# Optimization experiments

Hardware: AMD Instinct MI355X
Metric: run time of the kernel (lower is better)

Reference implementation:

```python
import jax, jax.numpy as jnp
import numpy as np

NEIGHBOR = 9
PAD = (NEIGHBOR - 1) // 2  # 4


def setup_inputs() -> dict:
    key = jax.random.key(0)
    k1, k2 = jax.random.split(key)
    B, C, H, W = 32, 3, 512, 512
    x = jax.random.normal(k1, (B, C, H, W), dtype=jnp.float32)
    p = jax.random.uniform(k2, (B, 1, H, W), dtype=jnp.float32)
    return {"x": x, "p": p}


def reference(x, p):
    # filter = ones(3, 3, 9, 9) / 9**2  (OIHW) — sums box mean over ALL 3 input
    # channels into each output channel, exactly as torch F.conv2d does here.
    filt = jnp.ones((3, 3, NEIGHBOR, NEIGHBOR), dtype=x.dtype) / (NEIGHBOR ** 2)
    mean_normal = jax.lax.conv_general_dilated(
        x, filt,
        window_strides=(1, 1),
        padding=[(PAD, PAD), (PAD, PAD)],
        dimension_numbers=("NCHW", "OIHW", "NCHW"),
    )
    return p * x + (1.0 - p) * mean_normal
```

## Files before the change

kernel.cpp:

```cpp
#include <hip/hip_runtime.h>


#define TX 64
#define TY 64
#define HALO 4
#define THW (TY + 2 * HALO)
#define TWW (TX + 2 * HALO)

__global__ __launch_bounds__(256) void reflection_fusion_kernel(
    const float* __restrict__ x, const float* __restrict__ p,
    float* __restrict__ out, int H, int W) {
  __shared__ __align__(16) float csum[THW][TWW];

  const int tid = threadIdx.x;
  const int b = blockIdx.z;
  const int x0 = blockIdx.x * TX;
  const int y0 = blockIdx.y * TY;
  const long HW = (long)H * W;
  const float* xb = x + (long)b * 3 * HW;
  const float* pb = p + (long)b * HW;
  float* ob = out + (long)b * 3 * HW;

  const int NCHUNK = THW * (TWW / 4);
#pragma unroll
  for (int pass = 0; pass < 6; ++pass) {
    int i = tid + pass * 256;
    if (i < NCHUNK) {
      int r = (unsigned)i / 18u;
      int j = i - r * 18;
      int gy = y0 + r - HALO;
      int gx = x0 + 4 * j - HALO;
      float4 s = make_float4(0.f, 0.f, 0.f, 0.f);
      if ((unsigned)gy < (unsigned)H && gx >= 0 && gx + 4 <= W) {
        const float* base = xb + (long)gy * W + gx;
        float4 a = *(const float4*)(base);
        float4 c1 = *(const float4*)(base + HW);
        float4 c2 = *(const float4*)(base + 2 * HW);
        s.x = a.x + c1.x + c2.x;
        s.y = a.y + c1.y + c2.y;
        s.z = a.z + c1.z + c2.z;
        s.w = a.w + c1.w + c2.w;
      }
      *(float4*)&csum[r][4 * j] = s;
    }
  }
  __syncthreads();

  const int cc = tid & 63;
  const int rg = tid >> 6;
  const int rbase = rg * 16;

  float h[24];
#pragma unroll
  for (int k = 0; k < 24; ++k) {
    const float* row = &csum[rbase + k][cc];
    float s = row[0];
#pragma unroll
    for (int d = 1; d < 9; ++d) s += row[d];
    h[k] = s;
  }

  const float inv81 = 1.0f / 81.0f;
  float s = 0.f;
#pragma unroll
  for (int k = 0; k < 9; ++k) s += h[k];

#pragma unroll
  for (int it = 0; it < 16; ++it) {
    if (it > 0) s += h[it + 8] - h[it - 1];
    int gy = y0 + rbase + it;
    long pix = (long)gy * W + (x0 + cc);
    float pv = pb[pix];
    float m = s * inv81;
    float om = 1.0f - pv;
    float v0 = xb[pix];
    float v1 = xb[HW + pix];
    float v2 = xb[2 * HW + pix];
    ob[pix] = pv * v0 + om * m;
    ob[HW + pix] = pv * v1 + om * m;
    ob[2 * HW + pix] = pv * v2 + om * m;
  }
}

extern "C" void kernel_launch(void* const* d_in, const int* in_sizes, int n_in,
                              void* d_out, int out_size, void* d_ws, size_t ws_size,
                              hipStream_t stream) {
  const float* x = (const float*)d_in[0];
  const float* p = (const float*)d_in[1];
  float* out = (float*)d_out;

  const int H = 512, W = 512;
  const int B = in_sizes[1] / (H * W);

  dim3 grid(W / TX, H / TY, B);
  dim3 block(256);
  reflection_fusion_kernel<<<grid, block, 0, stream>>>(x, p, out, H, W);
}
```

Measured before the change: 215.6 us.

## Use wide 256x16 tiles with float4 outputs and sliding horizontal box sums

The tile shape changes from 64x64 to 256 wide by 16 tall, and each thread now produces 4 adjacent columns over 4 rows instead of 1 column over 16 rows. Horizontal 9-tap sums are read as float4 from LDS and computed with a sliding window, and p, x and out are accessed with float4 global loads and stores. The aim is fewer global memory instructions, less LDS traffic and a cheaper horizontal sum. The cost is a larger relative halo (24 rows per 16 output rows), shorter vertical reuse, and 8-column left/right halo padding in LDS.

```diff
diff --git a/kernel.cpp b/kernel.cpp
--- a/kernel.cpp
+++ b/kernel.cpp
@@ -1,16 +1,15 @@
 #include <hip/hip_runtime.h>
 
 
-#define TX 64
-#define TY 64
-#define HALO 4
-#define THW (TY + 2 * HALO)
-#define TWW (TX + 2 * HALO)
+#define TX 256
+#define TY 16
+#define CROWS (TY + 8)
+#define CCOLS 272
 
 __global__ __launch_bounds__(256) void reflection_fusion_kernel(
     const float* __restrict__ x, const float* __restrict__ p,
     float* __restrict__ out, int H, int W) {
-  __shared__ __align__(16) float csum[THW][TWW];
+  __shared__ __align__(16) float csum[CROWS][CCOLS];
 
   const int tid = threadIdx.x;
   const int b = blockIdx.z;
@@ -21,64 +20,75 @@
   const float* pb = p + (long)b * HW;
   float* ob = out + (long)b * 3 * HW;
 
-  const int NCHUNK = THW * (TWW / 4);
-#pragma unroll
-  for (int pass = 0; pass < 6; ++pass) {
-    int i = tid + pass * 256;
-    if (i < NCHUNK) {
-      int r = (unsigned)i / 18u;
-      int j = i - r * 18;
-      int gy = y0 + r - HALO;
-      int gx = x0 + 4 * j - HALO;
-      float4 s = make_float4(0.f, 0.f, 0.f, 0.f);
-      if ((unsigned)gy < (unsigned)H && gx >= 0 && gx + 4 <= W) {
-        const float* base = xb + (long)gy * W + gx;
-        float4 a = *(const float4*)(base);
-        float4 c1 = *(const float4*)(base + HW);
-        float4 c2 = *(const float4*)(base + 2 * HW);
-        s.x = a.x + c1.x + c2.x;
-        s.y = a.y + c1.y + c2.y;
-        s.z = a.z + c1.z + c2.z;
-        s.w = a.w + c1.w + c2.w;
-      }
-      *(float4*)&csum[r][4 * j] = s;
+  for (int i = tid; i < CROWS * 68; i += 256) {
+    int r = (unsigned)i / 68u;
+    int k = i - r * 68;
+    int gy = y0 + r - 4;
+    int gx = x0 + 4 * k - 8;
+    float4 s = make_float4(0.f, 0.f, 0.f, 0.f);
+    if ((unsigned)gy < (unsigned)H && gx >= 0 && gx + 4 <= W) {
+      const float* base = xb + (long)gy * W + gx;
+      float4 a = *(const float4*)(base);
+      float4 c1 = *(const float4*)(base + HW);
+      float4 c2 = *(const float4*)(base + 2 * HW);
+      s.x = a.x + c1.x + c2.x;
+      s.y = a.y + c1.y + c2.y;
+      s.z = a.z + c1.z + c2.z;
+      s.w = a.w + c1.w + c2.w;
     }
+    *(float4*)&csum[r][4 * k] = s;
   }
   __syncthreads();
 
-  const int cc = tid & 63;
-  const int rg = tid >> 6;
-  const int rbase = rg * 16;
+  const int j = tid & 63;
+  const int r0 = (tid >> 6) << 2;
 
-  float h[24];
+  float h[12][4];
 #pragma unroll
-  for (int k = 0; k < 24; ++k) {
-    const float* row = &csum[rbase + k][cc];
-    float s = row[0];
-#pragma unroll
-    for (int d = 1; d < 9; ++d) s += row[d];
-    h[k] = s;
+  for (int i = 0; i < 12; ++i) {
+    const float* row = &csum[r0 + i][4 * j + 4];
+    float4 a = *(const float4*)(row);
+    float4 bq = *(const float4*)(row + 4);
+    float4 c = *(const float4*)(row + 8);
+    float s9 = ((a.x + a.y) + (a.z + a.w)) + ((bq.x + bq.y) + (bq.z + bq.w)) + c.x;
+    h[i][0] = s9;
+    s9 += c.y - a.x; h[i][1] = s9;
+    s9 += c.z - a.y; h[i][2] = s9;
+    s9 += c.w - a.z; h[i][3] = s9;
   }
 
   const float inv81 = 1.0f / 81.0f;
-  float s = 0.f;
+  float vs0 = 0.f, vs1 = 0.f, vs2 = 0.f, vs3 = 0.f;
 #pragma unroll
-  for (int k = 0; k < 9; ++k) s += h[k];
+  for (int i = 0; i < 9; ++i) {
+    vs0 += h[i][0]; vs1 += h[i][1]; vs2 += h[i][2]; vs3 += h[i][3];
+  }
 
 #pragma unroll
-  for (int it = 0; it < 16; ++it) {
-    if (it > 0) s += h[it + 8] - h[it - 1];
-    int gy = y0 + rbase + it;
-    long pix = (long)gy * W + (x0 + cc);
-    float pv = pb[pix];
-    float m = s * inv81;
-    float om = 1.0f - pv;
-    float v0 = xb[pix];
-    float v1 = xb[HW + pix];
-    float v2 = xb[2 * HW + pix];
-    ob[pix] = pv * v0 + om * m;
-    ob[HW + pix] = pv * v1 + om * m;
-    ob[2 * HW + pix] = pv * v2 + om * m;
+  for (int it = 0; it < 4; ++it) {
+    if (it > 0) {
+      vs0 += h[it + 8][0] - h[it - 1][0];
+      vs1 += h[it + 8][1] - h[it - 1][1];
+      vs2 += h[it + 8][2] - h[it - 1][2];
+      vs3 += h[it + 8][3] - h[it - 1][3];
+    }
+    int gy = y0 + r0 + it;
+    long pix = (long)gy * W + (x0 + 4 * j);
+    float4 pv = *(const float4*)(pb + pix);
+    float4 m = make_float4(vs0 * inv81, vs1 * inv81, vs2 * inv81, vs3 * inv81);
+    float4 om = make_float4(1.f - pv.x, 1.f - pv.y, 1.f - pv.z, 1.f - pv.w);
+    float4 t0 = make_float4(om.x * m.x, om.y * m.y, om.z * m.z, om.w * m.w);
+#pragma unroll
+    for (int c = 0; c < 3; ++c) {
+      const float* xs = xb + c * HW + pix;
+      float4 xv = *(const float4*)(xs);
+      float4 o;
+      o.x = pv.x * xv.x + t0.x;
+      o.y = pv.y * xv.y + t0.y;
+      o.z = pv.z * xv.z + t0.z;
+      o.w = pv.w * xv.w + t0.w;
+      *(float4*)(ob + c * HW + pix) = o;
+    }
   }
 }
 
```

After: 213.8 us. No clear change (-0.8%).
